# Kernel tuning notes

Hardware: AMD Instinct MI355X
Metric: run time of the kernel (lower is better)

## Reference

```python
import jax, jax.numpy as jnp
import numpy as np

B, T, N, H = 256, 128, 128, 256  # batch, window, n_input_series, encoder hidden


def setup_inputs() -> dict:
    key = jax.random.key(0)
    ks = jax.random.split(key, 11)
    s = 0.05
    return {
        "input_data": jax.random.normal(ks[0], (B, T, N), jnp.float32),
        # attn_layer_hidden: Linear(2H -> T)
        "W_ah": jax.random.normal(ks[1], (T, 2 * H), jnp.float32) * s,
        "b_ah": jax.random.normal(ks[2], (T,), jnp.float32) * s,
        # attn_layer_input: Linear(T -> 1)
        "W_ai": jax.random.normal(ks[3], (1, T), jnp.float32) * s,
        "b_ai": jax.random.normal(ks[4], (1,), jnp.float32) * s,
        # attn_layer: Linear(T -> 1)
        "W_a": jax.random.normal(ks[5], (1, T), jnp.float32) * s,
        "b_a": jax.random.normal(ks[6], (1,), jnp.float32) * s,
        # LSTM(N -> H), gate order i,f,g,o (PyTorch)
        "W_ih": jax.random.normal(ks[7], (4 * H, N), jnp.float32) * s,
        "W_hh": jax.random.normal(ks[8], (4 * H, H), jnp.float32) * s,
        "b_ih": jax.random.normal(ks[9], (4 * H,), jnp.float32) * s,
        "b_hh": jax.random.normal(ks[10], (4 * H,), jnp.float32) * s,
    }


def reference(input_data, W_ah, b_ah, W_ai, b_ai, W_a, b_a, W_ih, W_hh, b_ih, b_hh):
    b, t_len, n = input_data.shape
    h_dim = W_hh.shape[1]
    dt = input_data.dtype

    # attn_layer_input part is time-invariant: [B, N] (one scalar per series)
    ipart = jnp.einsum('btn,t->bn', input_data, W_ai[0]) + b_ai[0]

    xs = jnp.swapaxes(input_data, 0, 1)  # [T, B, N]

    def step(carry, x_t):
        h, c = carry  # each [B, H]
        hc = jnp.concatenate([h, c], axis=-1)          # [B, 2H]
        hpart = hc @ W_ah.T + b_ah                      # [B, T]
        z = jnp.tanh(hpart[:, None, :] + ipart[:, :, None])  # [B, N, T]
        score = jnp.einsum('bnt,t->bn', z, W_a[0]) + b_a[0]   # [B, N]
        attn = jax.nn.softmax(score, axis=-1)
        wx = attn * x_t                                 # weighted input [B, N]
        gates = wx @ W_ih.T + b_ih + h @ W_hh.T + b_hh  # [B, 4H]
        i, f, g, o = jnp.split(gates, 4, axis=-1)
        i = jax.nn.sigmoid(i)
        f = jax.nn.sigmoid(f)
        g = jnp.tanh(g)
        o = jax.nn.sigmoid(o)
        c2 = f * c + i * g
        h2 = o * jnp.tanh(c2)
        return (h2, c2), (wx, h2)

    h0 = jnp.zeros((b, h_dim), dt)
    c0 = jnp.zeros((b, h_dim), dt)
    (_, _), (iw, ie) = jax.lax.scan(step, (h0, c0), xs)
    input_weighted = jnp.swapaxes(iw, 0, 1)  # [B, T, N]
    input_encoded = jnp.swapaxes(ie, 0, 1)   # [B, T, H]
    return input_weighted, input_encoded
```

## Files before the change

kernel.cpp:

```cpp
#include <hip/hip_runtime.h>
#include <cstdint>

#define NB 256
#define NT 128
#define NS 128
#define NH 256
#define NTHR 1024
#define NWG  256
#define NGRP 64
#define GBAT 4
#define UPW  64

#define HC_OFF  0
#define CNT_OFF 131072

typedef _Float16 f16;
typedef _Float16 f16x2 __attribute__((ext_vector_type(2)));
typedef _Float16 f16x8 __attribute__((ext_vector_type(8)));
typedef float    f32x4 __attribute__((ext_vector_type(4)));

#define SW 528
#define SH 528
#define SA 136

__device__ __forceinline__ f16x2 pk(float a, float b) {
  f16x2 r; r.x = (f16)a; r.y = (f16)b; return r;
}
__device__ __forceinline__ f16x8 pack8(const float* s) {
  float4 v0 = *(const float4*)s, v1 = *(const float4*)(s + 4);
  f16x8 r;
  r[0] = (f16)v0.x; r[1] = (f16)v0.y; r[2] = (f16)v0.z; r[3] = (f16)v0.w;
  r[4] = (f16)v1.x; r[5] = (f16)v1.y; r[6] = (f16)v1.z; r[7] = (f16)v1.w;
  return r;
}
__device__ __forceinline__ void awr(uint32_t* p, uint32_t v) {
  __hip_atomic_store(p, v, __ATOMIC_RELAXED, __HIP_MEMORY_SCOPE_AGENT);
}
__device__ __forceinline__ uint32_t ard(uint32_t* p) {
  return __hip_atomic_load(p, __ATOMIC_RELAXED, __HIP_MEMORY_SCOPE_AGENT);
}
__device__ __forceinline__ void cinc(uint32_t* p) {
  __hip_atomic_fetch_add(p, 1u, __ATOMIC_RELAXED, __HIP_MEMORY_SCOPE_AGENT);
}
__device__ __forceinline__ void cwait(uint32_t* p, uint32_t tgt) {
  while (ard(p) < tgt) __builtin_amdgcn_s_sleep(1);
}

struct __align__(16) Sm {
  f16   wahp[128 * SW];
  f16   hcp[5 * SH];
  f16   act[5 * SA];
  float PW[4 * 128 * 2];
  float sp[2][4][128];
  float gacc[256][4];
  float gbias[256];
  float cbuf[64][4];
  float bah[128];
};

__global__ void enc_init(uint32_t* ws) {
  int i = blockIdx.x * blockDim.x + threadIdx.x;
  if (i < 65536) ws[HC_OFF + i] = 0u;
  if (i < 1024)  ws[CNT_OFF + i] = 0u;
}

__global__ __launch_bounds__(NTHR, 4) void enc_main(
    const float* __restrict__ x,    const float* __restrict__ W_ah,
    const float* __restrict__ b_ah, const float* __restrict__ W_ai,
    const float* __restrict__ b_ai, const float* __restrict__ W_a,
    const float* __restrict__ b_a,  const float* __restrict__ W_ih,
    const float* __restrict__ W_hh, const float* __restrict__ b_ih,
    const float* __restrict__ b_hh, float* __restrict__ out_iw,
    float* __restrict__ out_ie,     uint32_t* __restrict__ ws)
{
  __shared__ Sm sm;
  const int tid  = threadIdx.x;
  const int wg   = blockIdx.x;
  const int xcd  = wg & 7, slot = wg >> 3;
  const int g    = xcd * 8 + (slot >> 2);
  const int gid  = slot & 3;
  const int b0   = g * GBAT;
  const int u0   = gid * UPW;

  const int wv = tid >> 6, ln = tid & 63;
  const int bn = ln & 15, kq = ln >> 4;
  const int br = (bn < 4) ? bn : 4;

  uint32_t* cnt = ws + CNT_OFF + (size_t)g * 16;

  f16x8 wfrag[12];
  {
    const int lr = wv * 16 + bn;
    const int grow = (lr >> 6) * 256 + u0 + (lr & 63);
    #pragma unroll
    for (int kk = 0; kk < 4; ++kk)
      wfrag[kk] = pack8(W_ih + (size_t)grow * NS + kk * 32 + kq * 8);
    #pragma unroll
    for (int kk = 4; kk < 12; ++kk)
      wfrag[kk] = pack8(W_hh + (size_t)grow * NH + (kk - 4) * 32 + kq * 8);
  }

  #pragma unroll
  for (int i = 0; i < 8; ++i) {
    int idx = i * NTHR + tid;
    int r = idx >> 6, c = idx & 63;
    f16x8 v = pack8(W_ah + (size_t)r * 512 + c * 8);
    *(f16x8*)&sm.wahp[(size_t)r * SW + c * 8] = v;
  }
  if (tid < 256) {
    int grow = (tid >> 6) * 256 + u0 + (tid & 63);
    sm.gbias[tid] = b_ih[grow] + b_hh[grow];
    sm.cbuf[tid & 63][tid >> 6] = 0.f;
  }
  if (tid < 512) {
    int b = tid >> 7, tp = tid & 127;
    sm.PW[(b * 128 + tp) * 2 + 1] = 2.f * W_a[tp];
  }
  if (tid < 128) sm.bah[tid] = b_ah[tid];
  for (int i = tid; i < 5 * SH; i += NTHR) sm.hcp[i] = (f16)0.f;
  for (int i = tid; i < 5 * SA; i += NTHR) sm.act[i] = (f16)0.f;

  const int n_s = tid & 127, b_s = (tid >> 7) & 3, ts_s = tid >> 9;
  float ev;
  {
    const float* xb = x + (size_t)(b0 + b_s) * NT * NS;
    float a = 0.f;
    #pragma unroll 4
    for (int t = 0; t < NT; ++t) a = fmaf(xb[(size_t)t * NS + n_s], W_ai[t], a);
    ev = __expf(2.f * (a + b_ai[0]));
  }
  float S0;
  { float s = b_a[0]; for (int i = 0; i < 128; ++i) s += W_a[i]; S0 = s; }

  __syncthreads();

  for (int t = 0; t < NT; ++t) {
    const int par = t & 1, par2 = 1 - par;
    float xv0 = 0.f, xv1 = 0.f;
    if (wv < 4) {
      const float* xr = x + ((size_t)(b0 + wv) * NT + t) * NS;
      xv0 = xr[ln]; xv1 = xr[ln + 64];
    }
    if (t > 0) {
      if (tid == 0) cwait(cnt, 4u * (uint32_t)t);
      __syncthreads();
      {
        int b = tid >> 8, u = tid & 255;
        if ((u >> 6) != gid) {
          uint32_t v = ard(ws + HC_OFF + (((size_t)par * NGRP + g) * 4 + b) * 256 + u);
          f16x2 pv = __builtin_bit_cast(f16x2, v);
          sm.hcp[b * SH + u] = pv.x;
          sm.hcp[b * SH + 256 + u] = pv.y;
        }
      }
      __syncthreads();
    }
    if (wv < 8) {
      f32x4 acc = {0.f, 0.f, 0.f, 0.f};
      #pragma unroll
      for (int kk = 0; kk < 16; ++kk) {
        f16x8 a = *(const f16x8*)&sm.wahp[(size_t)(wv * 16 + bn) * SW + kk * 32 + kq * 8];
        f16x8 b = *(const f16x8*)&sm.hcp[(size_t)br * SH + kk * 32 + kq * 8];
        acc = __builtin_amdgcn_mfma_f32_16x16x32_f16(a, b, acc, 0, 0, 0);
      }
      if (bn < 4) {
        #pragma unroll
        for (int r = 0; r < 4; ++r) {
          int tp = wv * 16 + kq * 4 + r;
          sm.PW[(bn * 128 + tp) * 2] = __expf(2.f * (acc[r] + sm.bah[tp]));
        }
      }
    }
    __syncthreads();
    {
      float s = 0.f;
      #pragma unroll 8
      for (int i = 0; i < 32; ++i) {
        float4 rd = *(const float4*)&sm.PW[(b_s * 128 + ts_s * 64 + 2 * i) * 2];
        float d1 = fmaf(rd.x, ev, 1.f);
        float d2 = fmaf(rd.z, ev, 1.f);
        float num = fmaf(rd.w, d1, rd.y * d2);
        s = fmaf(num, __builtin_amdgcn_rcpf(d1 * d2), s);
      }
      sm.sp[ts_s][b_s][n_s] = s;
    }
    __syncthreads();
    if (wv < 4) {
      float sA = S0 - (sm.sp[0][wv][ln] + sm.sp[1][wv][ln]);
      float sB = S0 - (sm.sp[0][wv][ln + 64] + sm.sp[1][wv][ln + 64]);
      float m = fmaxf(sA, sB);
      #pragma unroll
      for (int o = 32; o; o >>= 1) m = fmaxf(m, __shfl_xor(m, o));
      float eA = __expf(sA - m), eB = __expf(sB - m);
      float ss = eA + eB;
      #pragma unroll
      for (int o = 32; o; o >>= 1) ss += __shfl_xor(ss, o);
      float rs = 1.f / ss;
      float wxA = eA * rs * xv0, wxB = eB * rs * xv1;
      sm.act[wv * SA + ln] = (f16)wxA;
      sm.act[wv * SA + ln + 64] = (f16)wxB;
      if (gid == wv) {
        float* ow = out_iw + ((size_t)(b0 + wv) * NT + t) * NS;
        ow[ln] = wxA; ow[ln + 64] = wxB;
      }
    }
    __syncthreads();
    {
      f32x4 acc = {0.f, 0.f, 0.f, 0.f};
      #pragma unroll
      for (int kk = 0; kk < 4; ++kk) {
        f16x8 a = *(const f16x8*)&sm.act[(size_t)br * SA + kk * 32 + kq * 8];
        acc = __builtin_amdgcn_mfma_f32_16x16x32_f16(a, wfrag[kk], acc, 0, 0, 0);
      }
      #pragma unroll
      for (int kk = 4; kk < 12; ++kk) {
        f16x8 a = *(const f16x8*)&sm.hcp[(size_t)br * SH + (kk - 4) * 32 + kq * 8];
        acc = __builtin_amdgcn_mfma_f32_16x16x32_f16(a, wfrag[kk], acc, 0, 0, 0);
      }
      if (ln < 16)
        *(f32x4*)&sm.gacc[wv * 16 + ln][0] = acc;
    }
    __syncthreads();
    if (tid < 256) {
      const int b = tid >> 6, ul = tid & 63;
      float gi = sm.gacc[ul][b]        + sm.gbias[ul];
      float gf = sm.gacc[64 + ul][b]   + sm.gbias[64 + ul];
      float gg = sm.gacc[128 + ul][b]  + sm.gbias[128 + ul];
      float go = sm.gacc[192 + ul][b]  + sm.gbias[192 + ul];
      float ii = 1.f / (1.f + __expf(-gi));
      float ff = 1.f / (1.f + __expf(-gf));
      float gt = 1.f - 2.f / (1.f + __expf(2.f * gg));
      float oo = 1.f / (1.f + __expf(-go));
      float c2 = ff * sm.cbuf[ul][b] + ii * gt;
      float h2 = oo * (1.f - 2.f / (1.f + __expf(2.f * c2)));
      sm.cbuf[ul][b] = c2;
      f16x2 pv = pk(h2, c2);
      sm.hcp[b * SH + u0 + ul] = pv.x;
      sm.hcp[b * SH + 256 + u0 + ul] = pv.y;
      out_ie[((size_t)(b0 + b) * NT + t) * NH + u0 + ul] = h2;
      awr(ws + HC_OFF + (((size_t)par2 * NGRP + g) * 4 + b) * 256 + u0 + ul,
          __builtin_bit_cast(uint32_t, pv));
    }
    __syncthreads();
    if (tid == 0) cinc(cnt);
  }
}

extern "C" void kernel_launch(void* const* d_in, const int* in_sizes, int n_in,
                              void* d_out, int out_size, void* d_ws, size_t ws_size,
                              hipStream_t stream) {
  const float* x    = (const float*)d_in[0];
  const float* W_ah = (const float*)d_in[1];
  const float* b_ah = (const float*)d_in[2];
  const float* W_ai = (const float*)d_in[3];
  const float* b_ai = (const float*)d_in[4];
  const float* W_a  = (const float*)d_in[5];
  const float* b_a  = (const float*)d_in[6];
  const float* W_ih = (const float*)d_in[7];
  const float* W_hh = (const float*)d_in[8];
  const float* b_ih = (const float*)d_in[9];
  const float* b_hh = (const float*)d_in[10];
  float* out_iw = (float*)d_out;
  float* out_ie = (float*)d_out + (size_t)NB * NT * NS;
  uint32_t* ws = (uint32_t*)d_ws;

  hipLaunchKernelGGL(enc_init, dim3(256), dim3(256), 0, stream, ws);
  hipLaunchKernelGGL(enc_main, dim3(NWG), dim3(NTHR), 0, stream,
                     x, W_ah, b_ah, W_ai, b_ai, W_a, b_a, W_ih, W_hh, b_ih, b_hh,
                     out_iw, out_ie, ws);
}
```

Measured before the change: 725.2 us.

## Halve batch per group to 2 and split attention over time slices across workgroups

Doubles the workgroup count to 512 with 2 batch rows per group instead of 4. Each of the 4 workgroups in a group now computes attention scores for only 32 of the 128 time positions, and the partial score sums are exchanged through global memory. A second per-step counter barrier is added for that exchange. This spreads the serial per-step work over more CUs, at the cost of an extra inter-workgroup synchronization per timestep and lower MFMA utilization, since only 2 of 16 columns are used.

```diff
diff --git a/kernel.cpp b/kernel.cpp
--- a/kernel.cpp
+++ b/kernel.cpp
@@ -6,13 +6,13 @@
 #define NS 128
 #define NH 256
 #define NTHR 1024
-#define NWG  256
-#define NGRP 64
-#define GBAT 4
-#define UPW  64
+#define NWG  512
+#define NGRP 128
 
 #define HC_OFF  0
-#define CNT_OFF 131072
+#define SP_OFF  131072
+#define CNT_OFF 262144
+#define WS_END  264192
 
 typedef _Float16 f16;
 typedef _Float16 f16x2 __attribute__((ext_vector_type(2)));
@@ -47,24 +47,24 @@
 }
 
 struct __align__(16) Sm {
-  f16   wahp[128 * SW];
-  f16   hcp[5 * SH];
-  f16   act[5 * SA];
-  float PW[4 * 128 * 2];
-  float sp[2][4][128];
-  float gacc[256][4];
+  f16   wahT[32 * SW];
+  f16   hcp[3 * SH];
+  f16   act[3 * SA];
+  float pacc[8][32][2];
+  float PW[2 * 32 * 2];
+  float spx[4][2][128];
+  float gacc[256][2];
   float gbias[256];
-  float cbuf[64][4];
-  float bah[128];
+  float cbuf[64][2];
+  float bah[32];
 };
 
 __global__ void enc_init(uint32_t* ws) {
-  int i = blockIdx.x * blockDim.x + threadIdx.x;
-  if (i < 65536) ws[HC_OFF + i] = 0u;
-  if (i < 1024)  ws[CNT_OFF + i] = 0u;
-}
-
-__global__ __launch_bounds__(NTHR, 4) void enc_main(
+  int i = blockIdx.x * 256 + threadIdx.x;
+  if (i < WS_END) ws[i] = 0u;
+}
+
+__global__ __launch_bounds__(NTHR, 8) void enc_main(
     const float* __restrict__ x,    const float* __restrict__ W_ah,
     const float* __restrict__ b_ah, const float* __restrict__ W_ai,
     const float* __restrict__ b_ai, const float* __restrict__ W_a,
@@ -77,16 +77,18 @@
   const int tid  = threadIdx.x;
   const int wg   = blockIdx.x;
   const int xcd  = wg & 7, slot = wg >> 3;
-  const int g    = xcd * 8 + (slot >> 2);
+  const int g    = xcd * 16 + (slot >> 2);
   const int gid  = slot & 3;
-  const int b0   = g * GBAT;
-  const int u0   = gid * UPW;
+  const int b0   = g * 2;
+  const int u0   = gid * 64;
+  const int tp0  = gid * 32;
 
   const int wv = tid >> 6, ln = tid & 63;
   const int bn = ln & 15, kq = ln >> 4;
-  const int br = (bn < 4) ? bn : 4;
-
-  uint32_t* cnt = ws + CNT_OFF + (size_t)g * 16;
+  const int br = (bn < 2) ? bn : 2;
+
+  uint32_t* cntH = ws + CNT_OFF + (size_t)g * 16 + 0;
+  uint32_t* cntS = ws + CNT_OFF + (size_t)g * 16 + 1;
 
   f16x8 wfrag[12];
   {
@@ -101,26 +103,26 @@
   }
 
   #pragma unroll
-  for (int i = 0; i < 8; ++i) {
+  for (int i = 0; i < 2; ++i) {
     int idx = i * NTHR + tid;
     int r = idx >> 6, c = idx & 63;
-    f16x8 v = pack8(W_ah + (size_t)r * 512 + c * 8);
-    *(f16x8*)&sm.wahp[(size_t)r * SW + c * 8] = v;
+    f16x8 v = pack8(W_ah + (size_t)(tp0 + r) * 512 + c * 8);
+    *(f16x8*)&sm.wahT[(size_t)r * SW + c * 8] = v;
   }
   if (tid < 256) {
     int grow = (tid >> 6) * 256 + u0 + (tid & 63);
     sm.gbias[tid] = b_ih[grow] + b_hh[grow];
-    sm.cbuf[tid & 63][tid >> 6] = 0.f;
-  }
-  if (tid < 512) {
-    int b = tid >> 7, tp = tid & 127;
-    sm.PW[(b * 128 + tp) * 2 + 1] = 2.f * W_a[tp];
-  }
-  if (tid < 128) sm.bah[tid] = b_ah[tid];
-  for (int i = tid; i < 5 * SH; i += NTHR) sm.hcp[i] = (f16)0.f;
-  for (int i = tid; i < 5 * SA; i += NTHR) sm.act[i] = (f16)0.f;
-
-  const int n_s = tid & 127, b_s = (tid >> 7) & 3, ts_s = tid >> 9;
+  }
+  if (tid < 64) {
+    int tl = tid >> 1, b = tid & 1;
+    sm.PW[(b * 32 + tl) * 2 + 1] = 2.f * W_a[tp0 + tl];
+  }
+  if (tid < 32) sm.bah[tid] = b_ah[tp0 + tid];
+  if (tid < 128) sm.cbuf[tid >> 1][tid & 1] = 0.f;
+  for (int i = tid; i < 3 * SH; i += NTHR) sm.hcp[i] = (f16)0.f;
+  for (int i = tid; i < 3 * SA; i += NTHR) sm.act[i] = (f16)0.f;
+
+  const int n_s = tid & 127, b_s = (tid >> 7) & 1;
   float ev;
   {
     const float* xb = x + (size_t)(b0 + b_s) * NT * NS;
@@ -137,57 +139,76 @@
   for (int t = 0; t < NT; ++t) {
     const int par = t & 1, par2 = 1 - par;
     float xv0 = 0.f, xv1 = 0.f;
-    if (wv < 4) {
+    if (wv < 2) {
       const float* xr = x + ((size_t)(b0 + wv) * NT + t) * NS;
       xv0 = xr[ln]; xv1 = xr[ln + 64];
     }
     if (t > 0) {
-      if (tid == 0) cwait(cnt, 4u * (uint32_t)t);
+      if (tid == 0) cwait(cntH, 4u * (uint32_t)t);
       __syncthreads();
-      {
-        int b = tid >> 8, u = tid & 255;
-        if ((u >> 6) != gid) {
-          uint32_t v = ard(ws + HC_OFF + (((size_t)par * NGRP + g) * 4 + b) * 256 + u);
-          f16x2 pv = __builtin_bit_cast(f16x2, v);
-          sm.hcp[b * SH + u] = pv.x;
-          sm.hcp[b * SH + 256 + u] = pv.y;
-        }
+      if (tid < 384) {
+        int b = tid / 192, j = tid % 192;
+        int u = (u0 + 64 + j) & 255;
+        uint32_t v = ard(ws + HC_OFF + (((size_t)par * NGRP + g) * 2 + b) * 256 + u);
+        f16x2 pv = __builtin_bit_cast(f16x2, v);
+        sm.hcp[b * SH + u] = pv.x;
+        sm.hcp[b * SH + 256 + u] = pv.y;
       }
       __syncthreads();
     }
-    if (wv < 8) {
+    {
+      const int tile = wv & 1, slice = wv >> 1;
       f32x4 acc = {0.f, 0.f, 0.f, 0.f};
       #pragma unroll
-      for (int kk = 0; kk < 16; ++kk) {
-        f16x8 a = *(const f16x8*)&sm.wahp[(size_t)(wv * 16 + bn) * SW + kk * 32 + kq * 8];
-        f16x8 b = *(const f16x8*)&sm.hcp[(size_t)br * SH + kk * 32 + kq * 8];
+      for (int kk = 0; kk < 2; ++kk) {
+        int kc = slice * 2 + kk;
+        f16x8 a = *(const f16x8*)&sm.wahT[(size_t)(tile * 16 + bn) * SW + kc * 32 + kq * 8];
+        f16x8 b = *(const f16x8*)&sm.hcp[(size_t)br * SH + kc * 32 + kq * 8];
         acc = __builtin_amdgcn_mfma_f32_16x16x32_f16(a, b, acc, 0, 0, 0);
       }
-      if (bn < 4) {
+      if (bn < 2) {
         #pragma unroll
-        for (int r = 0; r < 4; ++r) {
-          int tp = wv * 16 + kq * 4 + r;
-          sm.PW[(bn * 128 + tp) * 2] = __expf(2.f * (acc[r] + sm.bah[tp]));
-        }
-      }
-    }
-    __syncthreads();
-    {
+        for (int r = 0; r < 4; ++r)
+          sm.pacc[slice][tile * 16 + kq * 4 + r][bn] = acc[r];
+      }
+    }
+    __syncthreads();
+    if (tid < 64) {
+      int tl = tid >> 1, b = tid & 1;
+      float s = 0.f;
+      #pragma unroll
+      for (int sl = 0; sl < 8; ++sl) s += sm.pacc[sl][tl][b];
+      sm.PW[(b * 32 + tl) * 2] = __expf(2.f * (s + sm.bah[tl]));
+    }
+    __syncthreads();
+    if (tid < 256) {
+      const int b = tid >> 7, n = tid & 127;
       float s = 0.f;
       #pragma unroll 8
-      for (int i = 0; i < 32; ++i) {
-        float4 rd = *(const float4*)&sm.PW[(b_s * 128 + ts_s * 64 + 2 * i) * 2];
+      for (int i = 0; i < 16; ++i) {
+        float4 rd = *(const float4*)&sm.PW[(b * 32 + 2 * i) * 2];
         float d1 = fmaf(rd.x, ev, 1.f);
         float d2 = fmaf(rd.z, ev, 1.f);
         float num = fmaf(rd.w, d1, rd.y * d2);
         s = fmaf(num, __builtin_amdgcn_rcpf(d1 * d2), s);
       }
-      sm.sp[ts_s][b_s][n_s] = s;
-    }
-    __syncthreads();
-    if (wv < 4) {
-      float sA = S0 - (sm.sp[0][wv][ln] + sm.sp[1][wv][ln]);
-      float sB = S0 - (sm.sp[0][wv][ln + 64] + sm.sp[1][wv][ln + 64]);
+      awr(ws + SP_OFF + (((size_t)g * 4 + gid) * 2 + b) * 128 + n,
+          __builtin_bit_cast(uint32_t, s));
+    }
+    __syncthreads();
+    if (tid == 0) { cinc(cntS); cwait(cntS, 4u * (uint32_t)(t + 1)); }
+    __syncthreads();
+    {
+      int gq = tid >> 8, rem = tid & 255;
+      uint32_t v = ard(ws + SP_OFF + (((size_t)g * 4 + gq) * 2) * 128 + rem);
+      sm.spx[gq][rem >> 7][rem & 127] = __builtin_bit_cast(float, v);
+    }
+    __syncthreads();
+    if (wv < 2) {
+      float sA = S0 - (sm.spx[0][wv][ln] + sm.spx[1][wv][ln] +
+                       sm.spx[2][wv][ln] + sm.spx[3][wv][ln]);
+      float sB = S0 - (sm.spx[0][wv][ln + 64] + sm.spx[1][wv][ln + 64] +
+                       sm.spx[2][wv][ln + 64] + sm.spx[3][wv][ln + 64]);
       float m = fmaxf(sA, sB);
       #pragma unroll
       for (int o = 32; o; o >>= 1) m = fmaxf(m, __shfl_xor(m, o));
@@ -217,11 +238,10 @@
         f16x8 a = *(const f16x8*)&sm.hcp[(size_t)br * SH + (kk - 4) * 32 + kq * 8];
         acc = __builtin_amdgcn_mfma_f32_16x16x32_f16(a, wfrag[kk], acc, 0, 0, 0);
       }
-      if (ln < 16)
-        *(f32x4*)&sm.gacc[wv * 16 + ln][0] = acc;
-    }
-    __syncthreads();
-    if (tid < 256) {
+      if (ln < 16) { sm.gacc[wv * 16 + ln][0] = acc[0]; sm.gacc[wv * 16 + ln][1] = acc[1]; }
+    }
+    __syncthreads();
+    if (tid < 128) {
       const int b = tid >> 6, ul = tid & 63;
       float gi = sm.gacc[ul][b]        + sm.gbias[ul];
       float gf = sm.gacc[64 + ul][b]   + sm.gbias[64 + ul];
@@ -238,11 +258,11 @@
       sm.hcp[b * SH + u0 + ul] = pv.x;
       sm.hcp[b * SH + 256 + u0 + ul] = pv.y;
       out_ie[((size_t)(b0 + b) * NT + t) * NH + u0 + ul] = h2;
-      awr(ws + HC_OFF + (((size_t)par2 * NGRP + g) * 4 + b) * 256 + u0 + ul,
+      awr(ws + HC_OFF + (((size_t)par2 * NGRP + g) * 2 + b) * 256 + u0 + ul,
           __builtin_bit_cast(uint32_t, pv));
     }
     __syncthreads();
-    if (tid == 0) cinc(cnt);
+    if (tid == 0) cinc(cntH);
   }
 }
 
@@ -264,7 +284,7 @@
   float* out_ie = (float*)d_out + (size_t)NB * NT * NS;
   uint32_t* ws = (uint32_t*)d_ws;
 
-  hipLaunchKernelGGL(enc_init, dim3(256), dim3(256), 0, stream, ws);
+  hipLaunchKernelGGL(enc_init, dim3((WS_END + 255) / 256), dim3(256), 0, stream, ws);
   hipLaunchKernelGGL(enc_main, dim3(NWG), dim3(NTHR), 0, stream,
                      x, W_ah, b_ah, W_ai, b_ai, W_a, b_a, W_ih, W_hh, b_ih, b_hh,
                      out_iw, out_ie, ws);
```

Result: slower. 2.129 ms (+193.6%).

## Replace counter barrier with epoch-tagged 64-bit exchange and overlap recurrent MFMA with scoring

Applied to the files above, without the earlier changes.

Each workgroup now publishes its h/c pair together with the step number in one 64-bit atomic word. Consumers spin on each word's tag, which replaces the shared per-group counter, the fetch-add, one block barrier and the double-buffered parity. The h @ W_hh MFMA work is also moved earlier: waves 8-15 do it while waves 0-7 compute the hidden attention projection, and waves 0-7 do it while waves 8-15 compute the attention score sums. The score loop now runs on half the threads over the full window instead of splitting it in two, which lengthens that phase for those threads. Many threads now poll global memory instead of one, which adds memory traffic.

```diff
diff --git a/kernel.cpp b/kernel.cpp
--- a/kernel.cpp
+++ b/kernel.cpp
@@ -11,9 +11,6 @@
 #define GBAT 4
 #define UPW  64
 
-#define HC_OFF  0
-#define CNT_OFF 131072
-
 typedef _Float16 f16;
 typedef _Float16 f16x2 __attribute__((ext_vector_type(2)));
 typedef _Float16 f16x8 __attribute__((ext_vector_type(8)));
@@ -33,17 +30,11 @@
   r[4] = (f16)v1.x; r[5] = (f16)v1.y; r[6] = (f16)v1.z; r[7] = (f16)v1.w;
   return r;
 }
-__device__ __forceinline__ void awr(uint32_t* p, uint32_t v) {
+__device__ __forceinline__ void awr64(uint64_t* p, uint64_t v) {
   __hip_atomic_store(p, v, __ATOMIC_RELAXED, __HIP_MEMORY_SCOPE_AGENT);
 }
-__device__ __forceinline__ uint32_t ard(uint32_t* p) {
+__device__ __forceinline__ uint64_t ard64(uint64_t* p) {
   return __hip_atomic_load(p, __ATOMIC_RELAXED, __HIP_MEMORY_SCOPE_AGENT);
-}
-__device__ __forceinline__ void cinc(uint32_t* p) {
-  __hip_atomic_fetch_add(p, 1u, __ATOMIC_RELAXED, __HIP_MEMORY_SCOPE_AGENT);
-}
-__device__ __forceinline__ void cwait(uint32_t* p, uint32_t tgt) {
-  while (ard(p) < tgt) __builtin_amdgcn_s_sleep(1);
 }
 
 struct __align__(16) Sm {
@@ -51,7 +42,7 @@
   f16   hcp[5 * SH];
   f16   act[5 * SA];
   float PW[4 * 128 * 2];
-  float sp[2][4][128];
+  float sp[4][128];
   float gacc[256][4];
   float gbias[256];
   float cbuf[64][4];
@@ -59,9 +50,8 @@
 };
 
 __global__ void enc_init(uint32_t* ws) {
-  int i = blockIdx.x * blockDim.x + threadIdx.x;
-  if (i < 65536) ws[HC_OFF + i] = 0u;
-  if (i < 1024)  ws[CNT_OFF + i] = 0u;
+  int i = blockIdx.x * 256 + threadIdx.x;
+  if (i < 131072) ws[i] = 0u;
 }
 
 __global__ __launch_bounds__(NTHR, 4) void enc_main(
@@ -71,7 +61,7 @@
     const float* __restrict__ b_a,  const float* __restrict__ W_ih,
     const float* __restrict__ W_hh, const float* __restrict__ b_ih,
     const float* __restrict__ b_hh, float* __restrict__ out_iw,
-    float* __restrict__ out_ie,     uint32_t* __restrict__ ws)
+    float* __restrict__ out_ie,     uint64_t* __restrict__ hex)
 {
   __shared__ Sm sm;
   const int tid  = threadIdx.x;
@@ -85,8 +75,6 @@
   const int wv = tid >> 6, ln = tid & 63;
   const int bn = ln & 15, kq = ln >> 4;
   const int br = (bn < 4) ? bn : 4;
-
-  uint32_t* cnt = ws + CNT_OFF + (size_t)g * 16;
 
   f16x8 wfrag[12];
   {
@@ -120,7 +108,7 @@
   for (int i = tid; i < 5 * SH; i += NTHR) sm.hcp[i] = (f16)0.f;
   for (int i = tid; i < 5 * SA; i += NTHR) sm.act[i] = (f16)0.f;
 
-  const int n_s = tid & 127, b_s = (tid >> 7) & 3, ts_s = tid >> 9;
+  const int n_s = tid & 127, b_s = (tid >> 7) & 3;
   float ev;
   {
     const float* xb = x + (size_t)(b0 + b_s) * NT * NS;
@@ -135,26 +123,28 @@
   __syncthreads();
 
   for (int t = 0; t < NT; ++t) {
-    const int par = t & 1, par2 = 1 - par;
     float xv0 = 0.f, xv1 = 0.f;
     if (wv < 4) {
       const float* xr = x + ((size_t)(b0 + wv) * NT + t) * NS;
       xv0 = xr[ln]; xv1 = xr[ln + 64];
     }
     if (t > 0) {
-      if (tid == 0) cwait(cnt, 4u * (uint32_t)t);
+      if (tid < 768) {
+        int b = tid / 192, j = tid % 192;
+        int u = (u0 + 64 + j) & 255;
+        uint64_t* p = hex + ((size_t)g * 4 + b) * 256 + u;
+        uint64_t v = ard64(p);
+        while ((uint32_t)(v >> 32) != (uint32_t)t) {
+          __builtin_amdgcn_s_sleep(1);
+          v = ard64(p);
+        }
+        f16x2 pv = __builtin_bit_cast(f16x2, (uint32_t)v);
+        sm.hcp[b * SH + u] = pv.x;
+        sm.hcp[b * SH + 256 + u] = pv.y;
+      }
       __syncthreads();
-      {
-        int b = tid >> 8, u = tid & 255;
-        if ((u >> 6) != gid) {
-          uint32_t v = ard(ws + HC_OFF + (((size_t)par * NGRP + g) * 4 + b) * 256 + u);
-          f16x2 pv = __builtin_bit_cast(f16x2, v);
-          sm.hcp[b * SH + u] = pv.x;
-          sm.hcp[b * SH + 256 + u] = pv.y;
-        }
-      }
-      __syncthreads();
-    }
+    }
+    f32x4 accg = {0.f, 0.f, 0.f, 0.f};
     if (wv < 8) {
       f32x4 acc = {0.f, 0.f, 0.f, 0.f};
       #pragma unroll
@@ -170,24 +160,36 @@
           sm.PW[(bn * 128 + tp) * 2] = __expf(2.f * (acc[r] + sm.bah[tp]));
         }
       }
-    }
-    __syncthreads();
-    {
+    } else {
+      #pragma unroll
+      for (int kk = 4; kk < 12; ++kk) {
+        f16x8 a = *(const f16x8*)&sm.hcp[(size_t)br * SH + (kk - 4) * 32 + kq * 8];
+        accg = __builtin_amdgcn_mfma_f32_16x16x32_f16(a, wfrag[kk], accg, 0, 0, 0);
+      }
+    }
+    __syncthreads();
+    if (wv >= 8) {
+      const int b = (tid >> 7) & 3, n = tid & 127;
       float s = 0.f;
       #pragma unroll 8
-      for (int i = 0; i < 32; ++i) {
-        float4 rd = *(const float4*)&sm.PW[(b_s * 128 + ts_s * 64 + 2 * i) * 2];
+      for (int i = 0; i < 64; ++i) {
+        float4 rd = *(const float4*)&sm.PW[(b * 128 + 2 * i) * 2];
         float d1 = fmaf(rd.x, ev, 1.f);
         float d2 = fmaf(rd.z, ev, 1.f);
         float num = fmaf(rd.w, d1, rd.y * d2);
         s = fmaf(num, __builtin_amdgcn_rcpf(d1 * d2), s);
       }
-      sm.sp[ts_s][b_s][n_s] = s;
+      sm.sp[b][n] = S0 - s;
+    } else {
+      #pragma unroll
+      for (int kk = 4; kk < 12; ++kk) {
+        f16x8 a = *(const f16x8*)&sm.hcp[(size_t)br * SH + (kk - 4) * 32 + kq * 8];
+        accg = __builtin_amdgcn_mfma_f32_16x16x32_f16(a, wfrag[kk], accg, 0, 0, 0);
+      }
     }
     __syncthreads();
     if (wv < 4) {
-      float sA = S0 - (sm.sp[0][wv][ln] + sm.sp[1][wv][ln]);
-      float sB = S0 - (sm.sp[0][wv][ln + 64] + sm.sp[1][wv][ln + 64]);
+      float sA = sm.sp[wv][ln], sB = sm.sp[wv][ln + 64];
       float m = fmaxf(sA, sB);
       #pragma unroll
       for (int o = 32; o; o >>= 1) m = fmaxf(m, __shfl_xor(m, o));
@@ -206,19 +208,13 @@
     }
     __syncthreads();
     {
-      f32x4 acc = {0.f, 0.f, 0.f, 0.f};
       #pragma unroll
       for (int kk = 0; kk < 4; ++kk) {
         f16x8 a = *(const f16x8*)&sm.act[(size_t)br * SA + kk * 32 + kq * 8];
-        acc = __builtin_amdgcn_mfma_f32_16x16x32_f16(a, wfrag[kk], acc, 0, 0, 0);
-      }
-      #pragma unroll
-      for (int kk = 4; kk < 12; ++kk) {
-        f16x8 a = *(const f16x8*)&sm.hcp[(size_t)br * SH + (kk - 4) * 32 + kq * 8];
-        acc = __builtin_amdgcn_mfma_f32_16x16x32_f16(a, wfrag[kk], acc, 0, 0, 0);
+        accg = __builtin_amdgcn_mfma_f32_16x16x32_f16(a, wfrag[kk], accg, 0, 0, 0);
       }
       if (ln < 16)
-        *(f32x4*)&sm.gacc[wv * 16 + ln][0] = acc;
+        *(f32x4*)&sm.gacc[wv * 16 + ln][0] = accg;
     }
     __syncthreads();
     if (tid < 256) {
@@ -238,11 +234,11 @@
       sm.hcp[b * SH + u0 + ul] = pv.x;
       sm.hcp[b * SH + 256 + u0 + ul] = pv.y;
       out_ie[((size_t)(b0 + b) * NT + t) * NH + u0 + ul] = h2;
-      awr(ws + HC_OFF + (((size_t)par2 * NGRP + g) * 4 + b) * 256 + u0 + ul,
-          __builtin_bit_cast(uint32_t, pv));
-    }
-    __syncthreads();
-    if (tid == 0) cinc(cnt);
+      uint64_t pay = (uint64_t)__builtin_bit_cast(uint32_t, pv) |
+                     ((uint64_t)(uint32_t)(t + 1) << 32);
+      awr64(hex + ((size_t)g * 4 + b) * 256 + u0 + ul, pay);
+    }
+    __syncthreads();
   }
 }
 
@@ -262,10 +258,9 @@
   const float* b_hh = (const float*)d_in[10];
   float* out_iw = (float*)d_out;
   float* out_ie = (float*)d_out + (size_t)NB * NT * NS;
-  uint32_t* ws = (uint32_t*)d_ws;
-
-  hipLaunchKernelGGL(enc_init, dim3(256), dim3(256), 0, stream, ws);
+
+  hipLaunchKernelGGL(enc_init, dim3(512), dim3(256), 0, stream, (uint32_t*)d_ws);
   hipLaunchKernelGGL(enc_main, dim3(NWG), dim3(NTHR), 0, stream,
                      x, W_ah, b_ah, W_ai, b_ai, W_a, b_a, W_ih, W_hh, b_ih, b_hh,
-                     out_iw, out_ie, ws);
-}
+                     out_iw, out_ie, (uint64_t*)d_ws);
+}
```

Result: slower. 800.2 us (+10.4%).
